# Kernel tuning notes

Measured on AMD Instinct MI355X. Metric: run time of the kernel, lower is better.

Reference implementation:

```python
import jax, jax.numpy as jnp
import numpy as np
from jax import lax

NC1, NC2, NC3 = 64, 64, 512
TEMP = 1.0
EPS = 1e-5
B = 256


def setup_inputs() -> dict:
    key = jax.random.key(0)
    ks = jax.random.split(key, 16)
    d = {}
    d["inp"] = jax.random.normal(ks[0], (B, 3, 32, 32), jnp.float32)
    d["conv1_w"] = jax.random.normal(ks[1], (6, 3, 5, 5), jnp.float32) * 0.1
    d["conv1_b"] = jax.random.normal(ks[2], (6,), jnp.float32) * 0.1
    d["bn1_g"] = jnp.ones((6,), jnp.float32)
    d["bn1_b"] = jnp.zeros((6,), jnp.float32)
    d["conv2_w"] = jax.random.normal(ks[3], (16, 6, 5, 5), jnp.float32) * 0.1
    d["conv2_b"] = jax.random.normal(ks[4], (16,), jnp.float32) * 0.1
    d["bn2_g"] = jnp.ones((16,), jnp.float32)
    d["bn2_b"] = jnp.zeros((16,), jnp.float32)
    d["fc1_w"] = jax.random.normal(ks[5], (120, 400), jnp.float32) * 0.05
    d["fc1_b"] = jax.random.normal(ks[6], (120,), jnp.float32) * 0.05
    d["fc2_w"] = jax.random.normal(ks[7], (10, 120), jnp.float32) * 0.05
    d["fc2_b"] = jax.random.normal(ks[8], (10,), jnp.float32) * 0.05
    d["k1s"] = jax.random.normal(ks[9], (NC1, 6), jnp.float32)
    d["k2s"] = jax.random.normal(ks[10], (NC2, 16), jnp.float32)
    d["k3s"] = jax.random.normal(ks[11], (NC3, 120), jnp.float32)
    return d


def _conv(x, w, b):
    y = lax.conv_general_dilated(x, w, (1, 1), 'VALID',
                                 dimension_numbers=('NCHW', 'OIHW', 'NCHW'))
    return y + b[None, :, None, None]


def _bn_train(x, g, b):
    # BatchNorm2d in training mode: biased batch stats over (N,H,W)
    mean = x.mean(axis=(0, 2, 3), keepdims=True)
    var = ((x - mean) ** 2).mean(axis=(0, 2, 3), keepdims=True)
    return (x - mean) / jnp.sqrt(var + EPS) * g[None, :, None, None] + b[None, :, None, None]


def _maxpool2(x):
    return lax.reduce_window(x, -jnp.inf, lax.max, (1, 1, 2, 2), (1, 1, 2, 2), 'VALID')


def _codebook_logits_spatial(act, keys):
    # act: [B,C,H,W], keys: [K,C] -> -||act - k||_2 over C -> [B,K,H,W]
    diff = act[:, None] - keys[None, :, :, None, None]
    return -jnp.sqrt((diff ** 2).sum(axis=2))


def _neural_gas_loss(v, temp):
    n_clusters = v.shape[1]
    weightings = jnp.exp(-jnp.arange(n_clusters, dtype=v.dtype) / temp)
    sorted_v = jnp.sort(v, axis=1)
    return (sorted_v ** 2 * weightings).sum(axis=1)


def reference(inp, conv1_w, conv1_b, bn1_g, bn1_b, conv2_w, conv2_b, bn2_g, bn2_b,
              fc1_w, fc1_b, fc2_w, fc2_b, k1s, k2s, k3s):
    act1 = _bn_train(_conv(inp, conv1_w, conv1_b), bn1_g, bn1_b)          # [B,6,28,28]
    act_logits1 = _codebook_logits_spatial(act1, k1s)                     # [B,NC1,28,28]
    x = _maxpool2(jax.nn.relu(act1))                                      # [B,6,14,14]
    act2 = _bn_train(_conv(x, conv2_w, conv2_b), bn2_g, bn2_b)            # [B,16,10,10]
    act_logits2 = _codebook_logits_spatial(act2, k2s)                     # [B,NC2,10,10]
    x = _maxpool2(jax.nn.relu(act2))                                      # [B,16,5,5]
    x = x.reshape(x.shape[0], -1)                                         # [B,400]
    act3 = x @ fc1_w.T + fc1_b                                            # [B,120]
    diff3 = act3[:, None, :] - k3s[None, :, :]
    act_logits3 = -jnp.sqrt((diff3 ** 2).sum(axis=2))                     # [B,NC3]
    x = jax.nn.relu(act3)
    act4 = x @ fc2_w.T + fc2_b                                            # [B,10]
    # ARGS.ng branch: neural-gas cluster loss + argmax assignments
    cluster_loss = _neural_gas_loss(act_logits3, TEMP)                    # [B]
    assignments = jnp.argmax(act_logits3, axis=1)                         # [B] int
    return (assignments, cluster_loss.mean(), act4, act_logits1, act_logits2, act_logits3)
```

## Files before the change

kernel.cpp:

```cpp
#include <hip/hip_runtime.h>

#define B 256
#define EPSV 1e-5f

#define OFF_ASSIGN 0
#define OFF_LOSS   256
#define OFF_ACT4   257
#define OFF_L1     2817
#define OFF_L2     12847873
#define OFF_L3     14486273

__device__ __forceinline__ void wave_reduce2(float& s, float& q) {
#pragma unroll
    for (int o = 32; o > 0; o >>= 1) {
        s += __shfl_down(s, o, 64);
        q += __shfl_down(q, o, 64);
    }
}

__global__ __launch_bounds__(256) void conv1_kernel(
        const float* __restrict__ inp, const float* __restrict__ w,
        const float* __restrict__ bias, float* __restrict__ c1,
        float* __restrict__ part,
        const float* __restrict__ w1, const float* __restrict__ k3,
        float* __restrict__ w1t, float* __restrict__ k3st) {
    int bc = blockIdx.x;
    int tid = threadIdx.x;
    if (bc >= 1536) {
        int idx = (bc - 1536) * 256 + tid;
        if (idx < 48000) {
            int c = idx / 120, o = idx % 120;
            w1t[idx] = w1[o * 400 + c];
        } else if (idx < 48000 + 61440) {
            int j = idx - 48000;
            int c = j >> 9, k = j & 511;
            k3st[j] = k3[k * 120 + c];
        }
        return;
    }
    int b = bc / 6, c = bc % 6;
    __shared__ float ws[75];
    __shared__ float rs[4], rq[4];
    if (tid < 75) ws[tid] = w[c * 75 + tid];
    __syncthreads();
    const float* ip = inp + b * 3072;
    float bs = bias[c];
    float s = 0.f, sq = 0.f;
    for (int hw = tid; hw < 784; hw += 256) {
        int oh = hw / 28, ow = hw % 28;
        float acc = bs;
#pragma unroll
        for (int ic = 0; ic < 3; ++ic) {
            const float* ipc = ip + ic * 1024 + oh * 32 + ow;
            const float* wc = ws + ic * 25;
#pragma unroll
            for (int kh = 0; kh < 5; ++kh)
#pragma unroll
                for (int kw = 0; kw < 5; ++kw)
                    acc += ipc[kh * 32 + kw] * wc[kh * 5 + kw];
        }
        c1[bc * 784 + hw] = acc;
        s += acc; sq += acc * acc;
    }
    wave_reduce2(s, sq);
    if ((tid & 63) == 0) { rs[tid >> 6] = s; rq[tid >> 6] = sq; }
    __syncthreads();
    if (tid == 0) {
        part[bc * 2]     = rs[0] + rs[1] + rs[2] + rs[3];
        part[bc * 2 + 1] = rq[0] + rq[1] + rq[2] + rq[3];
    }
}

__global__ __launch_bounds__(1024) void stage1_kernel(
        const float* __restrict__ c1raw, const float* __restrict__ part1,
        const float* __restrict__ g1, const float* __restrict__ bb1,
        const float* __restrict__ k1s,
        const float* __restrict__ c2w, const float* __restrict__ c2b,
        float* __restrict__ out, float* __restrict__ c2raw,
        float* __restrict__ part2) {
    int b = blockIdx.x, tid = threadIdx.x;
    int lane = tid & 63, wid = tid >> 6;
    __shared__ __align__(16) float act[4704];
    __shared__ float sk1[384], k2sq1[64];
    __shared__ float w2s[2400];
    __shared__ float xp[1176];
    __shared__ __align__(16) float sa[1600];
    __shared__ float chs[6], chq[6], ssc[6], ssh[6];
    if (wid < 6) {
        float s = 0.f, q = 0.f;
#pragma unroll
        for (int j = 0; j < 4; ++j) {
            int bi = lane + 64 * j;
            s += part1[(bi * 6 + wid) * 2];
            q += part1[(bi * 6 + wid) * 2 + 1];
        }
        wave_reduce2(s, q);
        if (lane == 0) { chs[wid] = s; chq[wid] = q; }
    }
    if (tid >= 640 && tid < 1024) sk1[tid - 640] = k1s[tid - 640];
    for (int i = tid; i < 2400; i += 1024) w2s[i] = c2w[i];
    __syncthreads();
    if (tid < 6) {
        float m = chs[tid] * (1.f / 200704.f);
        float v = chq[tid] * (1.f / 200704.f) - m * m;
        float sc = g1[tid] * rsqrtf(v + EPSV);
        ssc[tid] = sc; ssh[tid] = bb1[tid] - m * sc;
    }
    if (tid >= 64 && tid < 128) {
        int k = tid - 64;
        float s = 0.f;
#pragma unroll
        for (int c = 0; c < 6; ++c) { float x = sk1[k * 6 + c]; s += x * x; }
        k2sq1[k] = s;
    }
    __syncthreads();
    for (int i = tid; i < 4704; i += 1024) {
        int c = i / 784;
        act[i] = c1raw[b * 4704 + i] * ssc[c] + ssh[c];
    }
    __syncthreads();
    if (tid < 784) {
        float a0 = act[tid], a1 = act[784 + tid], a2 = act[1568 + tid];
        float a3 = act[2352 + tid], a4 = act[3136 + tid], a5 = act[3920 + tid];
        float A2 = a0*a0 + a1*a1 + a2*a2 + a3*a3 + a4*a4 + a5*a5;
        float* op = out + OFF_L1 + (long)b * 50176 + tid;
#pragma unroll 4
        for (int k = 0; k < 64; ++k) {
            const float* kp = sk1 + k * 6;
            float dot = a0*kp[0] + a1*kp[1] + a2*kp[2] + a3*kp[3] + a4*kp[4] + a5*kp[5];
            *op = -sqrtf(fmaxf(A2 + k2sq1[k] - 2.f * dot, 0.f));
            op += 784;
        }
    } else {
        for (int i = tid - 784; i < 1176; i += 240) {
            int c = i / 196, p = i % 196, ph = p / 14, pw = p % 14;
            const float* ap = act + c * 784 + ph * 56 + pw * 2;
            float m = fmaxf(fmaxf(ap[0], ap[1]), fmaxf(ap[28], ap[29]));
            xp[i] = fmaxf(m, 0.f);
        }
    }
    __syncthreads();
    for (int i = tid; i < 1600; i += 1024) {
        int c = i / 100, hw = i - c * 100;
        int oh = hw / 10, ow = hw - oh * 10;
        float acc = c2b[c];
#pragma unroll
        for (int ic = 0; ic < 6; ++ic) {
            const float* xsrc = xp + ic * 196 + oh * 14 + ow;
            const float* wp = w2s + c * 150 + ic * 25;
#pragma unroll
            for (int kh = 0; kh < 5; ++kh)
#pragma unroll
                for (int kw = 0; kw < 5; ++kw)
                    acc += xsrc[kh * 14 + kw] * wp[kh * 5 + kw];
        }
        sa[i] = acc;
        c2raw[b * 1600 + i] = acc;
    }
    __syncthreads();
    {
        float s = 0.f, q = 0.f;
        if (lane < 100) { float x = sa[wid * 100 + lane]; s = x; q = x * x; }
        if (lane < 36)  { float x = sa[wid * 100 + 64 + lane]; s += x; q += x * x; }
        wave_reduce2(s, q);
        if (lane == 0) { part2[(b * 16 + wid) * 2] = s; part2[(b * 16 + wid) * 2 + 1] = q; }
    }
}

__global__ __launch_bounds__(1024) void stage2_kernel(
        const float* __restrict__ c2raw, const float* __restrict__ part2,
        const float* __restrict__ g2, const float* __restrict__ bb2,
        const float* __restrict__ k2s,
        const float* __restrict__ w1t, const float* __restrict__ f1b,
        const float* __restrict__ f2w, const float* __restrict__ f2b,
        const float* __restrict__ k3st,
        float* __restrict__ out, float* __restrict__ lossb) {
    int b = blockIdx.x, tid = threadIdx.x;
    int lane = tid & 63, wid = tid >> 6;
    __shared__ __align__(16) float sa[1600];
    __shared__ float sk2[1024], k2sq2[64];
    __shared__ float chs[16], chq[16], ssc[16], ssh[16];
    __shared__ float xs[400];
    __shared__ float partq[1024];
    __shared__ float a3r[120], a3p[120];
    __shared__ __align__(16) float sv[512];
    __shared__ __align__(16) float pv[1024];
    __shared__ int cntp[1024];
    __shared__ float wsum[8], wmv[8];
    __shared__ int wmi[8];
    {
        float s = 0.f, q = 0.f;
#pragma unroll
        for (int j = 0; j < 4; ++j) {
            int bi = lane + 64 * j;
            s += part2[(bi * 16 + wid) * 2];
            q += part2[(bi * 16 + wid) * 2 + 1];
        }
        wave_reduce2(s, q);
        if (lane == 0) { chs[wid] = s; chq[wid] = q; }
    }
    sk2[tid] = k2s[tid];
    __syncthreads();
    if (tid < 16) {
        float m = chs[tid] * (1.f / 25600.f);
        float v = chq[tid] * (1.f / 25600.f) - m * m;
        float sc = g2[tid] * rsqrtf(v + EPSV);
        ssc[tid] = sc; ssh[tid] = bb2[tid] - m * sc;
    }
    if (tid >= 64 && tid < 128) {
        int k = tid - 64;
        float s = 0.f;
#pragma unroll
        for (int c = 0; c < 16; ++c) { float x = sk2[k * 16 + c]; s += x * x; }
        k2sq2[k] = s;
    }
    __syncthreads();
    for (int i = tid; i < 1600; i += 1024) {
        int c = i / 100;
        sa[i] = c2raw[b * 1600 + i] * ssc[c] + ssh[c];
    }
    __syncthreads();
    if (tid < 800) {
        int kg = tid / 100, hw = tid - kg * 100;
        float a[16], A2 = 0.f;
#pragma unroll
        for (int c = 0; c < 16; ++c) { a[c] = sa[c * 100 + hw]; A2 += a[c] * a[c]; }
        float* op2 = out + OFF_L2 + (long)b * 6400 + kg * 800 + hw;
#pragma unroll
        for (int k = kg * 8; k < kg * 8 + 8; ++k) {
            const float* kp = sk2 + k * 16;
            float dot = 0.f;
#pragma unroll
            for (int c = 0; c < 16; ++c) dot += a[c] * kp[c];
            *op2 = -sqrtf(fmaxf(A2 + k2sq2[k] - 2.f * dot, 0.f));
            op2 += 100;
        }
    } else {
        for (int i = tid - 800; i < 400; i += 224) {
            int c = i / 25, p = i % 25, ph = p / 5, pw = p % 5;
            const float* ap = sa + c * 100 + ph * 20 + pw * 2;
            float m = fmaxf(fmaxf(ap[0], ap[1]), fmaxf(ap[10], ap[11]));
            xs[i] = fmaxf(m, 0.f);
        }
    }
    __syncthreads();
    {
        int o = tid & 127, q8 = tid >> 7;
        float s = 0.f;
        if (o < 120) {
            const float* wp = w1t + (q8 * 50) * 120 + o;
            const float* xq = xs + q8 * 50;
#pragma unroll 10
            for (int c = 0; c < 50; ++c) s += xq[c] * wp[c * 120];
        }
        partq[q8 * 128 + o] = s;
    }
    __syncthreads();
    if (tid < 120) {
        float acc = f1b[tid];
#pragma unroll
        for (int q8 = 0; q8 < 8; ++q8) acc += partq[q8 * 128 + tid];
        a3r[tid] = acc;
        a3p[tid] = fmaxf(acc, 0.f);
    }
    __syncthreads();
    {
        int k = tid & 511, h = tid >> 9;
        const float* kp = k3st + k;
        float s = 0.f;
#pragma unroll 6
        for (int c = h * 60; c < h * 60 + 60; ++c) {
            float d = a3r[c] - kp[c * 512];
            s += d * d;
        }
        pv[h * 512 + k] = s;
    }
    if (tid < 10) {
        float acc = f2b[tid];
        const float* wp = f2w + tid * 120;
#pragma unroll 8
        for (int c = 0; c < 120; ++c) acc += a3p[c] * wp[c];
        out[OFF_ACT4 + b * 10 + tid] = acc;
    }
    __syncthreads();
    if (tid < 512) {
        float v = -sqrtf(pv[tid] + pv[512 + tid]);
        sv[tid] = v;
        out[OFF_L3 + (long)b * 512 + tid] = v;
    }
    __syncthreads();
    {
        int i = tid & 511, h = tid >> 9;
        float v = sv[i];
        const float4* sv4 = reinterpret_cast<const float4*>(sv);
        int cnt = 0;
#pragma unroll 8
        for (int j4 = h * 64; j4 < h * 64 + 64; ++j4) {
            float4 o4 = sv4[j4];
            int jb = j4 * 4;
            cnt += (o4.x < v || (o4.x == v && jb < i)) ? 1 : 0;
            cnt += (o4.y < v || (o4.y == v && jb + 1 < i)) ? 1 : 0;
            cnt += (o4.z < v || (o4.z == v && jb + 2 < i)) ? 1 : 0;
            cnt += (o4.w < v || (o4.w == v && jb + 3 < i)) ? 1 : 0;
        }
        cntp[h * 512 + i] = cnt;
    }
    __syncthreads();
    if (tid < 512) {
        float v = sv[tid];
        int cnt = cntp[tid] + cntp[512 + tid];
        float contrib = v * v * expf(-(float)cnt);
        float ssum = contrib;
#pragma unroll
        for (int o = 32; o > 0; o >>= 1) ssum += __shfl_down(ssum, o, 64);
        float mv = v; int mi = tid;
#pragma unroll
        for (int o = 32; o > 0; o >>= 1) {
            float ov = __shfl_down(mv, o, 64);
            int oi = __shfl_down(mi, o, 64);
            if (ov > mv || (ov == mv && oi < mi)) { mv = ov; mi = oi; }
        }
        if (lane == 0) { wsum[wid] = ssum; wmv[wid] = mv; wmi[wid] = mi; }
    }
    __syncthreads();
    if (tid == 0) {
        float tot = 0.f;
        float bmv = wmv[0]; int bmi = wmi[0];
#pragma unroll
        for (int w = 0; w < 8; ++w) {
            tot += wsum[w];
            if (wmv[w] > bmv || (wmv[w] == bmv && wmi[w] < bmi)) { bmv = wmv[w]; bmi = wmi[w]; }
        }
        lossb[b] = tot;
        out[OFF_ASSIGN + b] = (float)bmi;
    }
}

__global__ void final_kernel(const float* __restrict__ loss_b, float* __restrict__ out_loss) {
    __shared__ float r[256];
    int tid = threadIdx.x;
    r[tid] = loss_b[tid];
    __syncthreads();
    for (int s = 128; s > 0; s >>= 1) {
        if (tid < s) r[tid] += r[tid + s];
        __syncthreads();
    }
    if (tid == 0) out_loss[0] = r[0] / 256.f;
}

extern "C" void kernel_launch(void* const* d_in, const int* in_sizes, int n_in,
                              void* d_out, int out_size, void* d_ws, size_t ws_size,
                              hipStream_t stream) {
    const float* inp = (const float*)d_in[0];
    const float* c1w = (const float*)d_in[1];
    const float* c1b = (const float*)d_in[2];
    const float* g1  = (const float*)d_in[3];
    const float* bb1 = (const float*)d_in[4];
    const float* c2w = (const float*)d_in[5];
    const float* c2b = (const float*)d_in[6];
    const float* g2  = (const float*)d_in[7];
    const float* bb2 = (const float*)d_in[8];
    const float* f1w = (const float*)d_in[9];
    const float* f1b = (const float*)d_in[10];
    const float* f2w = (const float*)d_in[11];
    const float* f2b = (const float*)d_in[12];
    const float* k1  = (const float*)d_in[13];
    const float* k2  = (const float*)d_in[14];
    const float* k3  = (const float*)d_in[15];
    float* out = (float*)d_out;

    float* W = (float*)d_ws;
    float* c1raw = W;
    float* part1 = c1raw + 1204224;
    float* c2raw = part1 + 3072;
    float* part2 = c2raw + 409600;
    float* lossb = part2 + 8192;
    float* w1t   = lossb + 256;
    float* k3st  = w1t + 48000;

    conv1_kernel<<<1964, 256, 0, stream>>>(inp, c1w, c1b, c1raw, part1,
                                           f1w, k3, w1t, k3st);
    stage1_kernel<<<B, 1024, 0, stream>>>(c1raw, part1, g1, bb1, k1, c2w, c2b,
                                          out, c2raw, part2);
    stage2_kernel<<<B, 1024, 0, stream>>>(c2raw, part2, g2, bb2, k2,
                                          w1t, f1b, f2w, f2b, k3st, out, lossb);
    final_kernel<<<1, 256, 0, stream>>>(lossb, out + OFF_LOSS);
}
```

Before: 91.79 us.

## Recompute conv1 in stage1, split codebook work per block, fold final reduction

The first kernel now only produces BatchNorm statistics. It no longer writes the full conv1 activation. Stage1 stages the input image in shared memory and recomputes conv1 itself, which removes a multi-megabyte write and read round trip through global memory. Stage1 also runs two blocks per sample, each emitting half of the 64 codebook distances, to raise parallelism. The final loss reduction moves into stage2 through an atomic last-block counter, which needs an added memset. The cost is conv1 computed three times per sample, redundant conv2 work and writes in both half-blocks, and an extra memset launch.

```diff
diff --git a/kernel.cpp b/kernel.cpp
--- a/kernel.cpp
+++ b/kernel.cpp
@@ -18,10 +18,9 @@
     }
 }
 
-__global__ __launch_bounds__(256) void conv1_kernel(
+__global__ __launch_bounds__(256) void conv1_stats_kernel(
         const float* __restrict__ inp, const float* __restrict__ w,
-        const float* __restrict__ bias, float* __restrict__ c1,
-        float* __restrict__ part,
+        const float* __restrict__ bias, float* __restrict__ part,
         const float* __restrict__ w1, const float* __restrict__ k3,
         float* __restrict__ w1t, float* __restrict__ k3st) {
     int bc = blockIdx.x;
@@ -59,7 +58,6 @@
                 for (int kw = 0; kw < 5; ++kw)
                     acc += ipc[kh * 32 + kw] * wc[kh * 5 + kw];
         }
-        c1[bc * 784 + hw] = acc;
         s += acc; sq += acc * acc;
     }
     wave_reduce2(s, sq);
@@ -71,21 +69,30 @@
     }
 }
 
-__global__ __launch_bounds__(1024) void stage1_kernel(
-        const float* __restrict__ c1raw, const float* __restrict__ part1,
+__global__ __launch_bounds__(1024, 8) void stage1_kernel(
+        const float* __restrict__ inp, const float* __restrict__ c1w,
+        const float* __restrict__ c1b, const float* __restrict__ part1,
         const float* __restrict__ g1, const float* __restrict__ bb1,
         const float* __restrict__ k1s,
         const float* __restrict__ c2w, const float* __restrict__ c2b,
         float* __restrict__ out, float* __restrict__ c2raw,
         float* __restrict__ part2) {
-    int b = blockIdx.x, tid = threadIdx.x;
+    int b = blockIdx.x >> 1, h = blockIdx.x & 1;
+    int tid = threadIdx.x;
     int lane = tid & 63, wid = tid >> 6;
+    __shared__ __align__(16) float si[3072];
     __shared__ __align__(16) float act[4704];
+    __shared__ float cw[450], cb1s[6];
     __shared__ float sk1[384], k2sq1[64];
     __shared__ float w2s[2400];
     __shared__ float xp[1176];
     __shared__ __align__(16) float sa[1600];
     __shared__ float chs[6], chq[6], ssc[6], ssh[6];
+    for (int i = tid; i < 3072; i += 1024) si[i] = inp[b * 3072 + i];
+    if (tid < 450) cw[tid] = c1w[tid];
+    if (tid >= 512 && tid < 518) cb1s[tid - 512] = c1b[tid - 512];
+    if (tid >= 640 && tid < 1024) sk1[tid - 640] = k1s[tid - 640];
+    for (int i = tid; i < 2400; i += 1024) w2s[i] = c2w[i];
     if (wid < 6) {
         float s = 0.f, q = 0.f;
 #pragma unroll
@@ -97,14 +104,12 @@
         wave_reduce2(s, q);
         if (lane == 0) { chs[wid] = s; chq[wid] = q; }
     }
-    if (tid >= 640 && tid < 1024) sk1[tid - 640] = k1s[tid - 640];
-    for (int i = tid; i < 2400; i += 1024) w2s[i] = c2w[i];
     __syncthreads();
     if (tid < 6) {
         float m = chs[tid] * (1.f / 200704.f);
         float v = chq[tid] * (1.f / 200704.f) - m * m;
         float sc = g1[tid] * rsqrtf(v + EPSV);
-        ssc[tid] = sc; ssh[tid] = bb1[tid] - m * sc;
+        ssc[tid] = sc; ssh[tid] = (cb1s[tid] - m) * sc + bb1[tid];
     }
     if (tid >= 64 && tid < 128) {
         int k = tid - 64;
@@ -115,17 +120,30 @@
     }
     __syncthreads();
     for (int i = tid; i < 4704; i += 1024) {
-        int c = i / 784;
-        act[i] = c1raw[b * 4704 + i] * ssc[c] + ssh[c];
+        int c = i / 784, hw = i - c * 784;
+        int oh = hw / 28, ow = hw - oh * 28;
+        float acc = 0.f;
+#pragma unroll
+        for (int ic = 0; ic < 3; ++ic) {
+            const float* ip = si + ic * 1024 + oh * 32 + ow;
+            const float* wp = cw + c * 75 + ic * 25;
+#pragma unroll
+            for (int kh = 0; kh < 5; ++kh)
+#pragma unroll
+                for (int kw = 0; kw < 5; ++kw)
+                    acc += ip[kh * 32 + kw] * wp[kh * 5 + kw];
+        }
+        act[i] = acc * ssc[c] + ssh[c];
     }
     __syncthreads();
     if (tid < 784) {
         float a0 = act[tid], a1 = act[784 + tid], a2 = act[1568 + tid];
         float a3 = act[2352 + tid], a4 = act[3136 + tid], a5 = act[3920 + tid];
         float A2 = a0*a0 + a1*a1 + a2*a2 + a3*a3 + a4*a4 + a5*a5;
-        float* op = out + OFF_L1 + (long)b * 50176 + tid;
+        float* op = out + OFF_L1 + (long)b * 50176 + (h * 32) * 784 + tid;
 #pragma unroll 4
-        for (int k = 0; k < 64; ++k) {
+        for (int kk = 0; kk < 32; ++kk) {
+            int k = h * 32 + kk;
             const float* kp = sk1 + k * 6;
             float dot = a0*kp[0] + a1*kp[1] + a2*kp[2] + a3*kp[3] + a4*kp[4] + a5*kp[5];
             *op = -sqrtf(fmaxf(A2 + k2sq1[k] - 2.f * dot, 0.f));
@@ -174,7 +192,8 @@
         const float* __restrict__ w1t, const float* __restrict__ f1b,
         const float* __restrict__ f2w, const float* __restrict__ f2b,
         const float* __restrict__ k3st,
-        float* __restrict__ out, float* __restrict__ lossb) {
+        float* __restrict__ out, float* __restrict__ lossb,
+        unsigned* __restrict__ done) {
     int b = blockIdx.x, tid = threadIdx.x;
     int lane = tid & 63, wid = tid >> 6;
     __shared__ __align__(16) float sa[1600];
@@ -188,6 +207,7 @@
     __shared__ int cntp[1024];
     __shared__ float wsum[8], wmv[8];
     __shared__ int wmi[8];
+    __shared__ int lastflag;
     {
         float s = 0.f, q = 0.f;
 #pragma unroll
@@ -333,19 +353,21 @@
         }
         lossb[b] = tot;
         out[OFF_ASSIGN + b] = (float)bmi;
-    }
-}
-
-__global__ void final_kernel(const float* __restrict__ loss_b, float* __restrict__ out_loss) {
-    __shared__ float r[256];
-    int tid = threadIdx.x;
-    r[tid] = loss_b[tid];
-    __syncthreads();
-    for (int s = 128; s > 0; s >>= 1) {
-        if (tid < s) r[tid] += r[tid + s];
+        __threadfence();
+        unsigned r = __hip_atomic_fetch_add(done, 1u, __ATOMIC_ACQ_REL, __HIP_MEMORY_SCOPE_AGENT);
+        lastflag = (r == (unsigned)(gridDim.x - 1)) ? 1 : 0;
+    }
+    __syncthreads();
+    if (lastflag) {
+        float* rf = pv;
+        if (tid < 256) rf[tid] = lossb[tid];
         __syncthreads();
-    }
-    if (tid == 0) out_loss[0] = r[0] / 256.f;
+        for (int s2 = 128; s2 > 0; s2 >>= 1) {
+            if (tid < s2) rf[tid] += rf[tid + s2];
+            __syncthreads();
+        }
+        if (tid == 0) out[OFF_LOSS] = rf[0] * (1.f / 256.f);
+    }
 }
 
 extern "C" void kernel_launch(void* const* d_in, const int* in_sizes, int n_in,
@@ -370,19 +392,19 @@
     float* out = (float*)d_out;
 
     float* W = (float*)d_ws;
-    float* c1raw = W;
-    float* part1 = c1raw + 1204224;
-    float* c2raw = part1 + 3072;
-    float* part2 = c2raw + 409600;
-    float* lossb = part2 + 8192;
-    float* w1t   = lossb + 256;
-    float* k3st  = w1t + 48000;
-
-    conv1_kernel<<<1964, 256, 0, stream>>>(inp, c1w, c1b, c1raw, part1,
-                                           f1w, k3, w1t, k3st);
-    stage1_kernel<<<B, 1024, 0, stream>>>(c1raw, part1, g1, bb1, k1, c2w, c2b,
-                                          out, c2raw, part2);
+    unsigned* done = (unsigned*)d_ws;
+    float* part1 = W + 64;
+    float* c2raw = W + 3136;
+    float* part2 = W + 412736;
+    float* lossb = W + 420928;
+    float* w1t   = W + 421184;
+    float* k3st  = W + 469184;
+
+    hipMemsetAsync(d_ws, 0, 64, stream);
+    conv1_stats_kernel<<<1964, 256, 0, stream>>>(inp, c1w, c1b, part1,
+                                                 f1w, k3, w1t, k3st);
+    stage1_kernel<<<B * 2, 1024, 0, stream>>>(inp, c1w, c1b, part1, g1, bb1, k1,
+                                              c2w, c2b, out, c2raw, part2);
     stage2_kernel<<<B, 1024, 0, stream>>>(c2raw, part2, g2, bb2, k2,
-                                          w1t, f1b, f2w, f2b, k3st, out, lossb);
-    final_kernel<<<1, 256, 0, stream>>>(lossb, out + OFF_LOSS);
+                                          w1t, f1b, f2w, f2b, k3st, out, lossb, done);
 }
```

Result: slower. 138.9 us (+51.3%).
